# Optimization experiments

Measured on AMD Instinct MI355X. Metric: run time of the kernel, lower is better.

## Reference

```python
import jax, jax.numpy as jnp
import numpy as np

B = 4096      # number of trees
DEPTH = 7     # complete binary tree depth -> N = 2**DEPTH - 1 = 127 nodes (heap order)
I_DIM = 300
H_DIM = 150


def setup_inputs() -> dict:
    key = jax.random.key(0)
    ks = jax.random.split(key, 6)
    N = 2 ** DEPTH - 1
    x = jax.random.normal(ks[0], (B, N, I_DIM), dtype=jnp.float32)
    Wiuo = jax.random.normal(ks[1], (3 * H_DIM, I_DIM), dtype=jnp.float32) / np.sqrt(I_DIM)
    Uiuo = jax.random.normal(ks[2], (3 * H_DIM, H_DIM), dtype=jnp.float32) / np.sqrt(H_DIM)
    biuo = jax.random.normal(ks[3], (1, 3 * H_DIM), dtype=jnp.float32) * 0.02
    Uf_w = jax.random.normal(ks[4], (H_DIM, H_DIM), dtype=jnp.float32) / np.sqrt(H_DIM)
    Uf_b = jax.random.normal(ks[5], (H_DIM,), dtype=jnp.float32) * 0.02
    return {"x": x, "Wiuo": Wiuo, "Uiuo": Uiuo, "biuo": biuo, "Uf_w": Uf_w, "Uf_b": Uf_b}


def reference(x, Wiuo, Uiuo, biuo, Uf_w, Uf_b):
    # Child-sum Tree-LSTM on complete binary trees (heap ordering).
    # Level d occupies node indices [2^d - 1, 2^(d+1) - 1); leaves at d = DEPTH-1.
    Bsz, N, _ = x.shape
    H = Uf_w.shape[0]
    # Input projection for all nodes (dropout in eval mode = identity)
    iuo_x = jnp.einsum('bni,ki->bnk', x, Wiuo)  # [B, N, 3H]
    h = jnp.zeros((Bsz, N, H), x.dtype)
    c = jnp.zeros((Bsz, N, H), x.dtype)
    for d in reversed(range(DEPTH)):  # leaves -> root (static loop over tree levels)
        start = 2 ** d - 1
        size = 2 ** d
        iuo = iuo_x[:, start:start + size]  # [B, size, 3H]
        if d == DEPTH - 1:
            c_sum = jnp.zeros((Bsz, size, H), x.dtype)
        else:
            cstart = 2 ** (d + 1) - 1
            ch = h[:, cstart:cstart + 2 * size].reshape(Bsz, size, 2, H)
            cc = c[:, cstart:cstart + 2 * size].reshape(Bsz, size, 2, H)
            h_tilda = ch.sum(axis=2)  # sum of children hidden states
            f = jax.nn.sigmoid(jnp.einsum('bskh,gh->bskg', ch, Uf_w) + Uf_b)
            c_sum = (f * cc).sum(axis=2)
            iuo = iuo + jnp.einsum('bsh,kh->bsk', h_tilda, Uiuo)
        iuo = iuo + biuo
        i_g, u_g, o_g = jnp.split(iuo, 3, axis=-1)
        c_new = jax.nn.sigmoid(i_g) * jnp.tanh(u_g) + c_sum
        h_new = jax.nn.sigmoid(o_g) * jnp.tanh(c_new)
        h = h.at[:, start:start + size].set(h_new)
        c = c.at[:, start:start + size].set(c_new)
    return h
```

## Files before the change

### kernel.cpp

```cpp
#include <hip/hip_runtime.h>

typedef float  f32x4  __attribute__((ext_vector_type(4)));
typedef short  s16x8  __attribute__((ext_vector_type(8)));
typedef short  s16x4  __attribute__((ext_vector_type(4)));
typedef _Float16 f16;

namespace {
constexpr int NN = 127, IDIM = 300, HD = 150;
constexpr int GNT = 512;
constexpr int LNT = 320;
constexpr int BCS = 36;
constexpr int SLAB_SH = 17408;
constexpr int SCH = 34;
constexpr int ASTR = 36;
constexpr int A_SH = 64 * ASTR;
constexpr int RSTR = 487;
constexpr int GEMM_LDS = (2*A_SH + 2*SLAB_SH) * 2;
constexpr int CSTR = 164;

constexpr int W_SH = 10 * SLAB_SH;
constexpr int U_SH = 480 * 160;
constexpr int F_SH = 160 * 160;

constexpr size_t C_N   = (size_t)4096 * 126 * HD;
constexpr size_t IUO_N = (size_t)4096 * 63 * 456;

__device__ __forceinline__ short f2bf(float f) {
    union { __bf16 b; short s; } u; u.b = (__bf16)f; return u.s;
}
__device__ __forceinline__ float bf2f(short s) {
    union { float f; unsigned u; } v; v.u = ((unsigned)(unsigned short)s) << 16; return v.f;
}
__device__ __forceinline__ short f2h_s(float f) {
    union { f16 h; short s; } u; u.h = (f16)f; return u.s;
}
__device__ __forceinline__ float h2f_s(short s) {
    union { f16 h; short s; } u; u.s = s; return (float)u.h;
}
__device__ __forceinline__ float sig_(float x)  { return 1.0f / (1.0f + __expf(-x)); }
__device__ __forceinline__ float tanh_(float x) { float e = __expf(2.0f * x); return 1.0f - 2.0f / (e + 1.0f); }
__device__ __forceinline__ s16x4 cvt4(float a,float b,float c,float d) {
    return s16x4{ f2bf(a), f2bf(b), f2bf(c), f2bf(d) };
}
__device__ __forceinline__ s16x8 cat(s16x4 lo, s16x4 hi) {
    return __builtin_shufflevector(lo, hi, 0,1,2,3,4,5,6,7);
}
__device__ __forceinline__ f32x4 MFMA(s16x8 a, s16x8 b, f32x4 c) {
    return __builtin_amdgcn_mfma_f32_16x16x32_bf16(a, b, c, 0, 0, 0);
}

typedef const __attribute__((address_space(1))) unsigned int* gp_t;
typedef __attribute__((address_space(3))) unsigned int* lp_t;
__device__ __forceinline__ void stage_slab(const short* g, short* l, int nch,
                                           int wv, int ln, int nw) {
    const char* gb = (const char*)g;
    char* lb = (char*)l;
    for (int c = wv; c < nch; c += nw)
        __builtin_amdgcn_global_load_lds((gp_t)(gb + c * 1024 + ln * 16),
                                         (lp_t)(lb + c * 1024 + ln * 16), 16, 0, 0);
}
}

__global__ __launch_bounds__(256)
void prep_w(const float* __restrict__ Wiuo, const float* __restrict__ Uiuo,
            const float* __restrict__ Ufw, short* __restrict__ dst) {
    int i = blockIdx.x * 256 + threadIdx.x;
    short v = 0;
    if (i < W_SH) {
        int kc = i / SLAB_SH, r = i - kc * SLAB_SH;
        if (r < 480 * BCS) {
            int col = r / BCS, j = r - col * BCS;
            int g = col / 160, cp = col - g * 160, k = kc * 32 + j;
            if (cp < HD && j < 32 && k < IDIM) v = f2bf(Wiuo[(size_t)(g*HD + cp)*IDIM + k]);
        }
        dst[i] = v;
    } else if (i < W_SH + U_SH) {
        int q = i - W_SH;
        int col = q / 160, k = q - col * 160;
        int g = col / 160, cp = col - g * 160;
        if (cp < HD && k < HD) v = f2bf(Uiuo[(size_t)(g*HD + cp)*HD + k]);
        dst[i] = v;
    } else if (i < W_SH + U_SH + F_SH) {
        int q = i - W_SH - U_SH;
        int col = q / 160, k = q - col * 160;
        if (col < HD && k < HD) v = f2bf(Ufw[(size_t)col*HD + k]);
        dst[i] = v;
    }
}

__global__ __launch_bounds__(GNT, 4)
void big_gemm(const float* __restrict__ x, const short* __restrict__ Wsl,
              const float* __restrict__ biuo, float* __restrict__ h_all,
              f16* __restrict__ c_all, f16* __restrict__ iuo_all)
{
    extern __shared__ short smem[];
    short* A0 = smem;
    short* A1 = A0 + A_SH;
    short* B0 = A1 + A_SH;
    short* B1 = B0 + SLAB_SH;
    short* rs = B0;

    const int t = threadIdx.x;
    const int wv = t >> 6, ln = t & 63, l15 = ln & 15, kg = ln >> 4;
    const int row0 = blockIdx.x * 64;

    int d = 6;
    for (int dd = 0; dd <= 5; ++dd)
        if (row0 >= 4096 * (128 - (2 << dd))) { d = dd; break; }
    const int base = 4096 * (128 - (2 << d));
    const int lg = d, mask = (1 << lg) - 1, start = (1 << lg) - 1;
    const int local0 = row0 - base;

    const int ar = t >> 3, aq = t & 7;
    const float* xrow;
    {
        int lcl = local0 + ar, b = lcl >> lg, s = lcl & mask;
        xrow = x + ((size_t)b * NN + start + s) * IDIM;
    }

    stage_slab(Wsl, B0, SCH, wv, ln, 8);
    {
        float4 f = *(const float4*)(xrow + aq * 4);
        *(s16x4*)&A0[ar * ASTR + aq * 4] = cvt4(f.x, f.y, f.z, f.w);
    }
    __syncthreads();

    f32x4 acc[4][4] = {};
    #pragma unroll
    for (int kc = 0; kc < 10; ++kc) {
        short* Ac = (kc & 1) ? A1 : A0;
        short* An = (kc & 1) ? A0 : A1;
        short* Bc = (kc & 1) ? B1 : B0;
        short* Bn = (kc & 1) ? B0 : B1;
        float4 nxt = {0.f, 0.f, 0.f, 0.f};
        if (kc < 9) {
            stage_slab(Wsl + (kc + 1) * SLAB_SH, Bn, SCH, wv, ln, 8);
            int k0 = (kc + 1) * 32 + aq * 4;
            if (k0 + 3 < IDIM) nxt = *(const float4*)(xrow + k0);
        }
        s16x8 a[4];
        #pragma unroll
        for (int mt = 0; mt < 4; ++mt) {
            const short* p = &Ac[(16*mt + l15) * ASTR + kg * 8];
            a[mt] = cat(*(const s16x4*)p, *(const s16x4*)(p + 4));
        }
        #pragma unroll
        for (int tt = 0; tt < 4; ++tt) {
            int ct = wv + 8 * tt;
            int cts = (ct < 30) ? ct : 29;
            const short* pb = &Bc[(cts * 16 + l15) * BCS + kg * 8];
            s16x8 bf = cat(*(const s16x4*)pb, *(const s16x4*)(pb + 4));
            #pragma unroll
            for (int mt = 0; mt < 4; ++mt)
                acc[tt][mt] = MFMA(a[mt], bf, acc[tt][mt]);
        }
        if (kc < 9) {
            *(s16x4*)&An[ar * ASTR + aq * 4] = cvt4(nxt.x, nxt.y, nxt.z, nxt.w);
            __syncthreads();
        }
    }

    if (d == 6) {
        __syncthreads();
        #pragma unroll
        for (int tt = 0; tt < 4; ++tt) {
            int ct = wv + 8 * tt;
            if (ct < 30) {
                #pragma unroll
                for (int mt = 0; mt < 4; ++mt)
                    #pragma unroll
                    for (int r = 0; r < 4; ++r)
                        rs[(16*mt + 4*kg + r) * RSTR + ct * 16 + l15] = f2h_s(acc[tt][mt][r]);
            }
        }
        __syncthreads();
        {
            int rr = t & 63, c0 = t >> 6;
            int lcl = local0 + rr, b = lcl >> 6, s = lcl & 63;
            const short* rp = &rs[rr * RSTR];
            size_t hb = ((size_t)b * NN + 63 + s) * HD;
            size_t cb = ((size_t)b * 126 + 62 + s) * HD;
            #pragma unroll
            for (int j = 0; j < 19; ++j) {
                int c = c0 + 8 * j;
                if (c < HD) {
                    float ig = h2f_s(rp[c])       + biuo[c];
                    float ug = h2f_s(rp[160 + c]) + biuo[HD + c];
                    float og = h2f_s(rp[320 + c]) + biuo[2*HD + c];
                    float cn = sig_(ig) * tanh_(ug);
                    float hn = sig_(og) * tanh_(cn);
                    h_all[hb + c] = hn;
                    c_all[cb + c] = (f16)cn;
                }
            }
        }
    } else {
        #pragma unroll
        for (int tt = 0; tt < 4; ++tt) {
            int ct = wv + 8 * tt;
            if (ct >= 30) continue;
            int g = ct / 10;
            int cig = (ct - g * 10) * 16 + l15;
            if (cig < HD) {
                #pragma unroll
                for (int mt = 0; mt < 4; ++mt)
                    #pragma unroll
                    for (int r = 0; r < 4; ++r) {
                        int lcl = local0 + 16*mt + 4*kg + r;
                        int b = lcl >> lg, s = lcl & mask;
                        iuo_all[((size_t)b*63 + start + s) * 456 + 152*g + cig] =
                            (f16)acc[tt][mt][r];
                    }
            }
        }
    }
}

__global__ __launch_bounds__(LNT, 4)
void lvl_light(const short* __restrict__ Ubf, const short* __restrict__ Fbf,
               const float* __restrict__ biuo, const float* __restrict__ Ufb,
               const f16* __restrict__ iuo_all, f16* __restrict__ c_all,
               float* __restrict__ h_all, int start, int lg, int cstart)
{
    __shared__ short chs[2][32][CSTR];
    __shared__ short fgs[5][64][34];

    const int t = threadIdx.x;
    const int wv = t >> 6, ln = t & 63, l15 = ln & 15, kg = ln >> 4;
    const int row0 = blockIdx.x * 32;
    const int mask = (1 << lg) - 1;
    int ct0 = 16 * (2*wv)     + l15;
    int ct1 = 16 * (2*wv + 1) + l15;

    {
        int rc = t & 63, part = t >> 6;
        int plane = rc >> 5, lr = rc & 31;
        int row = row0 + lr, b = row >> lg, s = row & mask;
        const float* hp = h_all + ((size_t)b*NN + cstart + 2*s + plane) * HD;
        short* dst = &chs[plane][lr][part * 32];
        #pragma unroll
        for (int q = 0; q < 8; ++q) {
            int k = part * 32 + q * 4;
            s16x4 v = {0,0,0,0};
            if (k + 3 < HD) {
                float4 f = *(const float4*)(hp + k);
                v = cvt4(f.x, f.y, f.z, f.w);
            } else if (k < HD) {
                float2 f = *(const float2*)(hp + k);
                v = s16x4{ f2bf(f.x), f2bf(f.y), 0, 0 };
            }
            *(s16x4*)(dst + q * 4) = v;
        }
    }
    __syncthreads();

    f32x4 facc[4][2] = {};
    #pragma unroll
    for (int kc = 0; kc < 5; ++kc) {
        int ka = kc * 32 + kg * 8;
        s16x8 af[4];
        #pragma unroll
        for (int rt = 0; rt < 4; ++rt) {
            const short* p = &chs[rt >> 1][(rt & 1) * 16 + l15][ka];
            af[rt] = cat(*(const s16x4*)p, *(const s16x4*)(p + 4));
        }
        #pragma unroll
        for (int tt = 0; tt < 2; ++tt) {
            int ct = tt ? ct1 : ct0;
            s16x8 bf = *(const s16x8*)(Fbf + (size_t)ct * 160 + ka);
            #pragma unroll
            for (int rt = 0; rt < 4; ++rt)
                facc[rt][tt] = MFMA(af[rt], bf, facc[rt][tt]);
        }
    }
    #pragma unroll
    for (int tt = 0; tt < 2; ++tt) {
        int ct = tt ? ct1 : ct0;
        float fb_ = (ct < HD) ? Ufb[ct] : 0.0f;
        #pragma unroll
        for (int rt = 0; rt < 4; ++rt)
            #pragma unroll
            for (int r = 0; r < 4; ++r)
                fgs[wv][rt*16 + 4*kg + r][tt*16 + l15] = f2bf(sig_(facc[rt][tt][r] + fb_));
    }
    __syncthreads();

    f32x4 acc[2][2][3] = {};
    #pragma unroll
    for (int kc = 0; kc < 5; ++kc) {
        int ka = kc * 32 + kg * 8;
        s16x8 hs[2];
        #pragma unroll
        for (int mt = 0; mt < 2; ++mt) {
            const short* p0 = &chs[0][16*mt + l15][ka];
            const short* p1 = &chs[1][16*mt + l15][ka];
            s16x8 h0 = cat(*(const s16x4*)p0, *(const s16x4*)(p0 + 4));
            s16x8 h1 = cat(*(const s16x4*)p1, *(const s16x4*)(p1 + 4));
            s16x8 hv;
            #pragma unroll
            for (int e = 0; e < 8; ++e)
                hv[e] = f2bf(bf2f(h0[e]) + bf2f(h1[e]));
            hs[mt] = hv;
        }
        #pragma unroll
        for (int tt = 0; tt < 2; ++tt) {
            int ct = tt ? ct1 : ct0;
            #pragma unroll
            for (int g = 0; g < 3; ++g) {
                s16x8 bf = *(const s16x8*)(Ubf + (size_t)(g*160 + ct) * 160 + ka);
                #pragma unroll
                for (int mt = 0; mt < 2; ++mt)
                    acc[mt][tt][g] = MFMA(hs[mt], bf, acc[mt][tt][g]);
            }
        }
    }

    #pragma unroll
    for (int tt = 0; tt < 2; ++tt) {
        int c = tt ? ct1 : ct0;
        if (c >= HD) continue;
        float bi = biuo[c], bu = biuo[HD + c], bo = biuo[2*HD + c];
        #pragma unroll
        for (int mt = 0; mt < 2; ++mt)
            #pragma unroll
            for (int r = 0; r < 4; ++r) {
                int pl = 16*mt + 4*kg + r;
                int row = row0 + pl, b = row >> lg, s = row & mask;
                const f16* ip = iuo_all + ((size_t)b*63 + start + s) * 456;
                float ig = (float)ip[c]       + bi + acc[mt][tt][0][r];
                float ug = (float)ip[152 + c] + bu + acc[mt][tt][1][r];
                float og = (float)ip[304 + c] + bo + acc[mt][tt][2][r];
                float f0 = bf2f(fgs[wv][pl][tt*16 + l15]);
                float f1 = bf2f(fgs[wv][32 + pl][tt*16 + l15]);
                size_t ci = (size_t)b*126 + (cstart + 2*s - 1);
                float c0 = (float)c_all[ci * HD + c];
                float c1 = (float)c_all[(ci + 1) * HD + c];
                float cn = sig_(ig) * tanh_(ug) + f0*c0 + f1*c1;
                float hn = sig_(og) * tanh_(cn);
                h_all[((size_t)b*NN + start + s) * HD + c] = hn;
                if (start > 0)
                    c_all[((size_t)b*126 + start + s - 1) * HD + c] = (f16)cn;
            }
    }
}

extern "C" void kernel_launch(void* const* d_in, const int* in_sizes, int n_in,
                              void* d_out, int out_size, void* d_ws, size_t ws_size,
                              hipStream_t stream) {
    const float* x    = (const float*)d_in[0];
    const float* Wiuo = (const float*)d_in[1];
    const float* Uiuo = (const float*)d_in[2];
    const float* biuo = (const float*)d_in[3];
    const float* Ufw  = (const float*)d_in[4];
    const float* Ufb  = (const float*)d_in[5];
    float* h = (float*)d_out;

    f16* c_all   = (f16*)d_ws;
    f16* iuo_all = c_all + C_N;
    short* slabs = (short*)(iuo_all + IUO_N);
    const short* Wsl = slabs;
    const short* Ubf = slabs + W_SH;
    const short* Fbf = slabs + W_SH + U_SH;

    (void)hipFuncSetAttribute((const void*)big_gemm,
                              hipFuncAttributeMaxDynamicSharedMemorySize, 160 * 1024);

    prep_w<<<(W_SH + U_SH + F_SH + 255) / 256, 256, 0, stream>>>(Wiuo, Uiuo, Ufw, slabs);

    big_gemm<<<8128, GNT, GEMM_LDS, stream>>>(x, Wsl, biuo, h, c_all, iuo_all);

    for (int d = 5; d >= 0; --d) {
        const int start = (1 << d) - 1, cstart = (1 << (d+1)) - 1;
        lvl_light<<<128 << d, LNT, 0, stream>>>(Ubf, Fbf, biuo, Ufb, iuo_all, c_all, h,
                                                start, d, cstart);
    }
}
```

Before: 1.227 ms.

## Load GEMM A operand directly from global into registers; precompute child h-sum in LDS

In big_gemm, the x tile is no longer staged through double-buffered LDS. Each lane loads its MFMA A fragments straight from global memory as float4 pairs and converts them to bf16 in registers, with loads interleaved between MFMA groups. This cuts LDS footprint and one barrier stage per k-chunk, at the cost of less-coalesced global reads of x and more registers per thread. In lvl_light, the child hidden-state sum is computed once into a new shared buffer rather than recomputed for every k-chunk and row tile in the Uiuo GEMM loop.

```diff
diff --git a/kernel.cpp b/kernel.cpp
--- a/kernel.cpp
+++ b/kernel.cpp
@@ -12,10 +12,8 @@
 constexpr int BCS = 36;
 constexpr int SLAB_SH = 17408;
 constexpr int SCH = 34;
-constexpr int ASTR = 36;
-constexpr int A_SH = 64 * ASTR;
 constexpr int RSTR = 487;
-constexpr int GEMM_LDS = (2*A_SH + 2*SLAB_SH) * 2;
+constexpr int GEMM_LDS = 2 * SLAB_SH * 2;
 constexpr int CSTR = 164;
 
 constexpr int W_SH = 10 * SLAB_SH;
@@ -44,6 +42,9 @@
 }
 __device__ __forceinline__ s16x8 cat(s16x4 lo, s16x4 hi) {
     return __builtin_shufflevector(lo, hi, 0,1,2,3,4,5,6,7);
+}
+__device__ __forceinline__ s16x8 cvt8f(float4 lo, float4 hi) {
+    return cat(cvt4(lo.x,lo.y,lo.z,lo.w), cvt4(hi.x,hi.y,hi.z,hi.w));
 }
 __device__ __forceinline__ f32x4 MFMA(s16x8 a, s16x8 b, f32x4 c) {
     return __builtin_amdgcn_mfma_f32_16x16x32_bf16(a, b, c, 0, 0, 0);
@@ -94,14 +95,11 @@
               f16* __restrict__ c_all, f16* __restrict__ iuo_all)
 {
     extern __shared__ short smem[];
-    short* A0 = smem;
-    short* A1 = A0 + A_SH;
-    short* B0 = A1 + A_SH;
-    short* B1 = B0 + SLAB_SH;
-    short* rs = B0;
+    short* rs = smem;
 
     const int t = threadIdx.x;
     const int wv = t >> 6, ln = t & 63, l15 = ln & 15, kg = ln >> 4;
+    const int kg8 = kg * 8;
     const int row0 = blockIdx.x * 64;
 
     int d = 6;
@@ -111,52 +109,56 @@
     const int lg = d, mask = (1 << lg) - 1, start = (1 << lg) - 1;
     const int local0 = row0 - base;
 
-    const int ar = t >> 3, aq = t & 7;
-    const float* xrow;
-    {
-        int lcl = local0 + ar, b = lcl >> lg, s = lcl & mask;
-        xrow = x + ((size_t)b * NN + start + s) * IDIM;
-    }
-
-    stage_slab(Wsl, B0, SCH, wv, ln, 8);
-    {
-        float4 f = *(const float4*)(xrow + aq * 4);
-        *(s16x4*)&A0[ar * ASTR + aq * 4] = cvt4(f.x, f.y, f.z, f.w);
-    }
-    __syncthreads();
+    const float* xr[4];
+    #pragma unroll
+    for (int mt = 0; mt < 4; ++mt) {
+        int lcl = local0 + 16*mt + l15, b = lcl >> lg, s = lcl & mask;
+        xr[mt] = x + ((size_t)b * NN + start + s) * IDIM + kg8;
+    }
+
+    stage_slab(Wsl, smem, SCH, wv, ln, 8);
 
     f32x4 acc[4][4] = {};
     #pragma unroll
     for (int kc = 0; kc < 10; ++kc) {
-        short* Ac = (kc & 1) ? A1 : A0;
-        short* An = (kc & 1) ? A0 : A1;
-        short* Bc = (kc & 1) ? B1 : B0;
-        short* Bn = (kc & 1) ? B0 : B1;
-        float4 nxt = {0.f, 0.f, 0.f, 0.f};
-        if (kc < 9) {
-            stage_slab(Wsl + (kc + 1) * SLAB_SH, Bn, SCH, wv, ln, 8);
-            int k0 = (kc + 1) * 32 + aq * 4;
-            if (k0 + 3 < IDIM) nxt = *(const float4*)(xrow + k0);
-        }
-        s16x8 a[4];
-        #pragma unroll
-        for (int mt = 0; mt < 4; ++mt) {
-            const short* p = &Ac[(16*mt + l15) * ASTR + kg * 8];
-            a[mt] = cat(*(const s16x4*)p, *(const s16x4*)(p + 4));
-        }
+        __syncthreads();
+        if (kc < 9)
+            stage_slab(Wsl + (kc+1)*SLAB_SH, smem + ((kc+1)&1)*SLAB_SH, SCH, wv, ln, 8);
+        const short* Bc = smem + (kc & 1) * SLAB_SH;
+        const int kb = kc * 32;
+        const bool v0 = (kb + kg8 + 4 <= IDIM);
+        const bool v1 = (kb + kg8 + 8 <= IDIM);
+        const float4 z = {0.f, 0.f, 0.f, 0.f};
+
+        s16x8 bf[4];
         #pragma unroll
         for (int tt = 0; tt < 4; ++tt) {
             int ct = wv + 8 * tt;
             int cts = (ct < 30) ? ct : 29;
-            const short* pb = &Bc[(cts * 16 + l15) * BCS + kg * 8];
-            s16x8 bf = cat(*(const s16x4*)pb, *(const s16x4*)(pb + 4));
-            #pragma unroll
-            for (int mt = 0; mt < 4; ++mt)
-                acc[tt][mt] = MFMA(a[mt], bf, acc[tt][mt]);
-        }
-        if (kc < 9) {
-            *(s16x4*)&An[ar * ASTR + aq * 4] = cvt4(nxt.x, nxt.y, nxt.z, nxt.w);
-            __syncthreads();
+            const short* pb = &Bc[(cts * 16 + l15) * BCS + kg8];
+            bf[tt] = cat(*(const s16x4*)pb, *(const s16x4*)(pb + 4));
+        }
+        float4 lo0 = v0 ? *(const float4*)(xr[0] + kb)     : z;
+        float4 hi0 = v1 ? *(const float4*)(xr[0] + kb + 4) : z;
+        float4 lo1 = v0 ? *(const float4*)(xr[1] + kb)     : z;
+        float4 hi1 = v1 ? *(const float4*)(xr[1] + kb + 4) : z;
+        s16x8 a0 = cvt8f(lo0, hi0);
+        s16x8 a1 = cvt8f(lo1, hi1);
+        float4 lo2 = v0 ? *(const float4*)(xr[2] + kb)     : z;
+        float4 hi2 = v1 ? *(const float4*)(xr[2] + kb + 4) : z;
+        float4 lo3 = v0 ? *(const float4*)(xr[3] + kb)     : z;
+        float4 hi3 = v1 ? *(const float4*)(xr[3] + kb + 4) : z;
+        #pragma unroll
+        for (int tt = 0; tt < 4; ++tt) {
+            acc[tt][0] = MFMA(a0, bf[tt], acc[tt][0]);
+            acc[tt][1] = MFMA(a1, bf[tt], acc[tt][1]);
+        }
+        s16x8 a2 = cvt8f(lo2, hi2);
+        s16x8 a3 = cvt8f(lo3, hi3);
+        #pragma unroll
+        for (int tt = 0; tt < 4; ++tt) {
+            acc[tt][2] = MFMA(a2, bf[tt], acc[tt][2]);
+            acc[tt][3] = MFMA(a3, bf[tt], acc[tt][3]);
         }
     }
 
@@ -223,6 +225,7 @@
                float* __restrict__ h_all, int start, int lg, int cstart)
 {
     __shared__ short chs[2][32][CSTR];
+    __shared__ short hts[32][CSTR];
     __shared__ short fgs[5][64][34];
 
     const int t = threadIdx.x;
@@ -254,6 +257,23 @@
     }
     __syncthreads();
 
+    {
+        int r = t / 10, seg = t - 10 * r;
+        int k0 = seg * 16;
+        s16x8 h0a = *(const s16x8*)&chs[0][r][k0];
+        s16x8 h0b = *(const s16x8*)&chs[0][r][k0 + 8];
+        s16x8 h1a = *(const s16x8*)&chs[1][r][k0];
+        s16x8 h1b = *(const s16x8*)&chs[1][r][k0 + 8];
+        s16x8 oa, ob;
+        #pragma unroll
+        for (int e = 0; e < 8; ++e) {
+            oa[e] = f2bf(bf2f(h0a[e]) + bf2f(h1a[e]));
+            ob[e] = f2bf(bf2f(h0b[e]) + bf2f(h1b[e]));
+        }
+        *(s16x8*)&hts[r][k0]     = oa;
+        *(s16x8*)&hts[r][k0 + 8] = ob;
+    }
+
     f32x4 facc[4][2] = {};
     #pragma unroll
     for (int kc = 0; kc < 5; ++kc) {
@@ -292,15 +312,8 @@
         s16x8 hs[2];
         #pragma unroll
         for (int mt = 0; mt < 2; ++mt) {
-            const short* p0 = &chs[0][16*mt + l15][ka];
-            const short* p1 = &chs[1][16*mt + l15][ka];
-            s16x8 h0 = cat(*(const s16x4*)p0, *(const s16x4*)(p0 + 4));
-            s16x8 h1 = cat(*(const s16x4*)p1, *(const s16x4*)(p1 + 4));
-            s16x8 hv;
-            #pragma unroll
-            for (int e = 0; e < 8; ++e)
-                hv[e] = f2bf(bf2f(h0[e]) + bf2f(h1[e]));
-            hs[mt] = hv;
+            const short* p = &hts[16*mt + l15][ka];
+            hs[mt] = cat(*(const s16x4*)p, *(const s16x4*)(p + 4));
         }
         #pragma unroll
         for (int tt = 0; tt < 2; ++tt) {
```

Measured after the change: 1.679 ms. 1.37x slower.
